# Kernel optimization log

Hardware: AMD Instinct MI355X
Metric: run time of the kernel (lower is better)

The kernel has to match this reference:

```python
import jax, jax.numpy as jnp
import numpy as np

N_TREES, N_LEAVES, PATH_LEN, N_NODES, D, B = 10, 16, 5, 31, 256, 4096


def _local_paths():
    # root-to-leaf paths of a full binary tree, depth 4: 31 nodes, 16 leaves, path len 5
    return np.array([[0, 1 + l // 8, 3 + l // 4, 7 + l // 2, 15 + l]
                     for l in range(N_LEAVES)], np.int32)


def setup_inputs() -> dict:
    key = jax.random.key(0)
    k1, k2, k3, k4, k5, k6 = jax.random.split(key, 6)
    # one activated leaf per tree -> multi-hot cross_features (B, N_TREES*N_LEAVES)
    leaf = jax.random.randint(k1, (B, N_TREES), 0, N_LEAVES)
    cross = jnp.zeros((B, N_TREES, N_LEAVES), jnp.float32)
    cross = cross.at[jnp.arange(B)[:, None], jnp.arange(N_TREES)[None, :], leaf].set(1.0)
    cross_features = cross.reshape(B, N_TREES * N_LEAVES)
    # learned params: node embedding table + single-layer LSTM (torch init scale 1/sqrt(D))
    emb = jax.random.normal(k2, (N_TREES * N_NODES, D), jnp.float32) * 0.02
    s = 1.0 / np.sqrt(D)
    W_ih = jax.random.uniform(k3, (4 * D, D), jnp.float32, -s, s)
    W_hh = jax.random.uniform(k4, (4 * D, D), jnp.float32, -s, s)
    b_ih = jax.random.uniform(k5, (4 * D,), jnp.float32, -s, s)
    b_hh = jax.random.uniform(k6, (4 * D,), jnp.float32, -s, s)
    return {"cross_features": cross_features, "emb": emb, "W_ih": W_ih,
            "W_hh": W_hh, "b_ih": b_ih, "b_hh": b_hh}


def reference(cross_features, emb, W_ih, W_hh, b_ih, b_hh):
    # global path node ids per (tree, leaf): [T, L, P]
    gpaths = jnp.asarray(_local_paths())[None, :, :] + \
        (jnp.arange(N_TREES, dtype=jnp.int32) * N_NODES)[:, None, None]
    # activated leaf per tree (exactly one hot per 16-leaf block)
    leaf = jnp.argmax(cross_features.reshape(B, N_TREES, N_LEAVES), axis=-1)  # [B, T]
    node_ids = gpaths[jnp.arange(N_TREES)[None, :], leaf]                     # [B, T, P]
    x = emb[node_ids].reshape(B * N_TREES, PATH_LEN, D)                       # packed paths
    # precompute input projections for all steps: [N, P, 4D]
    xg = jnp.einsum('npd,gd->npg', x, W_ih) + (b_ih + b_hh)

    def step(carry, xt):
        h, c = carry
        g = xt + h @ W_hh.T
        i, f, gg, o = jnp.split(g, 4, axis=-1)  # torch gate order: i, f, g, o
        c = jax.nn.sigmoid(f) * c + jax.nn.sigmoid(i) * jnp.tanh(gg)
        h = jax.nn.sigmoid(o) * jnp.tanh(c)
        return (h, c), None

    n = B * N_TREES
    h0 = jnp.zeros((n, D), x.dtype)
    (h, _), _ = jax.lax.scan(step, (h0, h0), jnp.swapaxes(xg, 0, 1))
    return h.reshape(B, N_TREES, D)
```

## Files before the change

### kernel.cpp

```cpp
#include <hip/hip_runtime.h>

#define NT 10
#define NL 16
#define NN 31
#define DD 256
#define G4 1024
#define NNODES (NT*NN)
#define NPATH (NT*NL)
#define NB 4096
#define NROWS (NB*NT)


__device__ __forceinline__ float sigf(float x)   { return 1.0f / (1.0f + __expf(-x)); }
__device__ __forceinline__ float tanh_f(float x) { return 2.0f / (1.0f + __expf(-2.0f*x)) - 1.0f; }

__global__ __launch_bounds__(256) void k_nodeproj(
    const float* __restrict__ emb, const float* __restrict__ Wih,
    const float* __restrict__ bih, const float* __restrict__ bhh,
    float* __restrict__ xg)
{
    __shared__ float smem[20 * 260 + 20 * 4 * 64];
    float4* es4 = (float4*)smem;
    float*  ps  = smem + 20 * 260;

    const int tid = threadIdx.x;
    const int nt  = blockIdx.x & 15;
    const int mt  = blockIdx.x >> 4;
    const int kq  = tid >> 6;
    const int w   = tid & 63;

    const float4* W4 = (const float4*)Wih + (size_t)(nt * 64 + w) * 64 + kq * 16;
    float4 wreg[16];
    #pragma unroll
    for (int j = 0; j < 16; ++j) wreg[j] = W4[j];

    const float4* emb4 = (const float4*)emb;
    #pragma unroll
    for (int r = 0; r < 5; ++r) {
        int idx = tid + 256 * r;
        int m = idx >> 6, q = idx & 63;
        int n = mt * 20 + m;
        es4[m * 65 + q] = (n < NNODES) ? emb4[(size_t)n * 64 + q]
                                       : make_float4(0.f, 0.f, 0.f, 0.f);
    }
    __syncthreads();

    float acc[20];
    #pragma unroll
    for (int m = 0; m < 20; ++m) acc[m] = 0.f;
    #pragma unroll
    for (int j = 0; j < 16; ++j) {
        float4 wv = wreg[j];
        #pragma unroll
        for (int m = 0; m < 20; ++m) {
            float4 h = es4[m * 65 + kq * 16 + j];
            acc[m] = fmaf(wv.x, h.x, fmaf(wv.y, h.y,
                     fmaf(wv.z, h.z, fmaf(wv.w, h.w, acc[m]))));
        }
    }
    #pragma unroll
    for (int m = 0; m < 20; ++m) ps[(m * 4 + kq) * 64 + w] = acc[m];
    __syncthreads();

    const int nl   = tid & 63;
    const int msub = tid >> 6;
    const int j    = nt * 64 + nl;
    const float bsum = bih[j] + bhh[j];
    #pragma unroll
    for (int r = 0; r < 5; ++r) {
        int m = msub * 5 + r;
        int n = mt * 20 + m;
        float s = ps[(m * 4 + 0) * 64 + nl] + ps[(m * 4 + 1) * 64 + nl]
                + ps[(m * 4 + 2) * 64 + nl] + ps[(m * 4 + 3) * 64 + nl];
        if (n < NNODES) xg[(size_t)n * G4 + j] = s + bsum;
    }
}

template<int SI, bool FIRST>
__global__ __launch_bounds__(256) void k_step(
    const float* __restrict__ xg, const float* __restrict__ Whh,
    const float* __restrict__ h_in, float* __restrict__ h_out,
    float* __restrict__ cB)
{
    __shared__ float smem[10 * 260 + 10 * 4 * 64];
    float4* hs4 = (float4*)smem;
    float*  hs  = smem;
    float*  ps  = smem + 10 * 260;

    const int tid   = threadIdx.x;
    const int pg    = blockIdx.x >> 4;
    const int dtile = blockIdx.x & 15;
    const int kq    = tid >> 6;
    const int w     = tid & 63;
    const int gate  = w >> 4;
    const int dlw   = w & 15;

    const float4* W4 = (const float4*)Whh
        + (size_t)(gate * 256 + dtile * 16 + dlw) * 64 + kq * 16;
    float4 wreg[16];
    #pragma unroll
    for (int j = 0; j < 16; ++j) wreg[j] = W4[j];

    if (FIRST) {
        #pragma unroll
        for (int r = 0; r < 10; ++r) {
            int p = r;
            int k = tid;
            int t = (pg * 10 + p) >> 4;
            const float* xr = xg + (size_t)(t * NN) * G4;
            float c1 = sigf(xr[k]) * tanh_f(xr[512 + k]);
            float h1 = sigf(xr[768 + k]) * tanh_f(c1);
            hs[p * 260 + k] = h1;
        }
    } else {
        const float4* hin4 = (const float4*)h_in;
        #pragma unroll
        for (int r = 0; r < 3; ++r) {
            int idx = tid + 256 * r;
            if (idx < 640)
                hs4[(idx >> 6) * 65 + (idx & 63)] = hin4[(size_t)pg * 640 + idx];
        }
    }
    __syncthreads();

    float acc[10];
    #pragma unroll
    for (int p = 0; p < 10; ++p) acc[p] = 0.f;
    #pragma unroll
    for (int j = 0; j < 16; ++j) {
        float4 wv = wreg[j];
        #pragma unroll
        for (int p = 0; p < 10; ++p) {
            float4 h = hs4[p * 65 + kq * 16 + j];
            acc[p] = fmaf(wv.x, h.x, fmaf(wv.y, h.y,
                     fmaf(wv.z, h.z, fmaf(wv.w, h.w, acc[p]))));
        }
    }
    #pragma unroll
    for (int p = 0; p < 10; ++p) ps[(p * 4 + kq) * 64 + w] = acc[p];
    __syncthreads();

    if (tid < 160) {
        const int p  = tid >> 4;
        const int dl = tid & 15;
        const int d  = dtile * 16 + dl;
        const int pglob = pg * 10 + p;
        const int t = pglob >> 4, l = pglob & 15;
        int off;
        if      (SI == 1) off = 1  + (l >> 3);
        else if (SI == 2) off = 3  + (l >> 2);
        else if (SI == 3) off = 7  + (l >> 1);
        else              off = 15 + l;
        const float* xn = xg + (size_t)(t * NN + off) * G4;

        float g0 = 0.f, g1 = 0.f, g2 = 0.f, g3 = 0.f;
        #pragma unroll
        for (int q = 0; q < 4; ++q) {
            g0 += ps[(p * 4 + q) * 64 +  0 + dl];
            g1 += ps[(p * 4 + q) * 64 + 16 + dl];
            g2 += ps[(p * 4 + q) * 64 + 32 + dl];
            g3 += ps[(p * 4 + q) * 64 + 48 + dl];
        }
        float c_in;
        if (FIRST) {
            int tt = pglob >> 4;
            const float* xr = xg + (size_t)(tt * NN) * G4;
            c_in = sigf(xr[d]) * tanh_f(xr[512 + d]);
        } else {
            c_in = cB[(size_t)pglob * DD + d];
        }
        float gi = g0 + xn[d];
        float gf = g1 + xn[256 + d];
        float gg = g2 + xn[512 + d];
        float go = g3 + xn[768 + d];
        float cn = sigf(gf) * c_in + sigf(gi) * tanh_f(gg);
        float hn = sigf(go) * tanh_f(cn);
        cB[(size_t)pglob * DD + d]    = cn;
        h_out[(size_t)pglob * DD + d] = hn;
    }
}

__global__ __launch_bounds__(256) void k_scatter(
    const float* __restrict__ cross, const float* __restrict__ htab,
    float* __restrict__ out)
{
    const int tid  = threadIdx.x;
    const int wave = tid >> 6;
    const int lane = tid & 63;
    const int r = blockIdx.x * 4 + wave;
    const int b = r / NT;
    const int t = r - b * NT;

    float v = 0.f;
    if (lane < NL) v = cross[(size_t)b * (NT * NL) + t * NL + lane];
    unsigned long long m = __ballot(v > 0.5f);
    int leaf = m ? (int)__builtin_ctzll(m) : 0;
    int p = t * NL + leaf;

    const float4* h4 = (const float4*)htab;
    float4* o4 = (float4*)out;
    o4[(size_t)r * 64 + lane] = h4[(size_t)p * 64 + lane];
}

extern "C" void kernel_launch(void* const* d_in, const int* in_sizes, int n_in,
                              void* d_out, int out_size, void* d_ws, size_t ws_size,
                              hipStream_t stream)
{
    const float* cross = (const float*)d_in[0];
    const float* emb   = (const float*)d_in[1];
    const float* Wih   = (const float*)d_in[2];
    const float* Whh   = (const float*)d_in[3];
    const float* bih   = (const float*)d_in[4];
    const float* bhh   = (const float*)d_in[5];
    float* out = (float*)d_out;

    float* ws = (float*)d_ws;
    float* xg = ws;
    float* hA = xg + NNODES * G4;
    float* hB = hA + NPATH * DD;
    float* cB = hB + NPATH * DD;

    hipLaunchKernelGGL(k_nodeproj, dim3(256), dim3(256), 0, stream,
                       emb, Wih, bih, bhh, xg);
    hipLaunchKernelGGL((k_step<1, true>),  dim3(256), dim3(256), 0, stream,
                       xg, Whh, hA, hA, cB);
    hipLaunchKernelGGL((k_step<2, false>), dim3(256), dim3(256), 0, stream,
                       xg, Whh, hA, hB, cB);
    hipLaunchKernelGGL((k_step<3, false>), dim3(256), dim3(256), 0, stream,
                       xg, Whh, hB, hA, cB);
    hipLaunchKernelGGL((k_step<4, false>), dim3(256), dim3(256), 0, stream,
                       xg, Whh, hA, hB, cB);
    hipLaunchKernelGGL(k_scatter, dim3(10240), dim3(256), 0, stream,
                       cross, hB, out);
}
```

Measured before the change: 125.9 us.

## Fuse node projection, LSTM steps and scatter into one cooperative kernel

Replaces the six separate launches (input projection, four recurrent steps, output gather) with a single cooperative persistent kernel of 256 blocks. Phases are separated by a hand-written grid barrier built on per-block arrival counters and a generation counter. W_hh is loaded into registers once, and the cell state stays in a register across steps instead of round-tripping through global memory. This is meant to remove launch gaps and redundant weight reloads between steps, at the cost of spin-wait barrier latency and a gather done by fewer blocks.

```diff
diff --git a/kernel.cpp b/kernel.cpp
--- a/kernel.cpp
+++ b/kernel.cpp
@@ -9,197 +9,217 @@
 #define NPATH (NT*NL)
 #define NB 4096
 #define NROWS (NB*NT)
-
+#define NBLK 256
+
+__device__ unsigned long long g_gen;
+__device__ unsigned long long g_arr[NBLK];
 
 __device__ __forceinline__ float sigf(float x)   { return 1.0f / (1.0f + __expf(-x)); }
 __device__ __forceinline__ float tanh_f(float x) { return 2.0f / (1.0f + __expf(-2.0f*x)) - 1.0f; }
 
-__global__ __launch_bounds__(256) void k_nodeproj(
-    const float* __restrict__ emb, const float* __restrict__ Wih,
-    const float* __restrict__ bih, const float* __restrict__ bhh,
-    float* __restrict__ xg)
+__device__ __forceinline__ void gbar(int bid, int tid, unsigned long long tgt,
+                                     volatile int* s_nd)
+{
+    __syncthreads();
+    if (tid == 0)
+        __hip_atomic_store(&g_arr[bid], tgt, __ATOMIC_RELEASE, __HIP_MEMORY_SCOPE_AGENT);
+    if (bid == 0) {
+        int nd = 1;
+        while (nd) {
+            if (tid == 0) *s_nd = 0;
+            __syncthreads();
+            unsigned long long v =
+                __hip_atomic_load(&g_arr[tid], __ATOMIC_RELAXED, __HIP_MEMORY_SCOPE_AGENT);
+            if (v < tgt) *s_nd = 1;
+            __syncthreads();
+            nd = *s_nd;
+            __syncthreads();
+            if (nd) __builtin_amdgcn_s_sleep(1);
+        }
+        __builtin_amdgcn_fence(__ATOMIC_ACQUIRE, "agent");
+        if (tid == 0)
+            __hip_atomic_store(&g_gen, tgt, __ATOMIC_RELEASE, __HIP_MEMORY_SCOPE_AGENT);
+    } else {
+        if (tid == 0) {
+            while (__hip_atomic_load(&g_gen, __ATOMIC_RELAXED, __HIP_MEMORY_SCOPE_AGENT) < tgt)
+                __builtin_amdgcn_s_sleep(1);
+            __builtin_amdgcn_fence(__ATOMIC_ACQUIRE, "agent");
+        }
+        __syncthreads();
+    }
+}
+
+__global__ __launch_bounds__(256) void k_fused(
+    const float* __restrict__ cross, const float* __restrict__ emb,
+    const float* __restrict__ Wih,   const float* __restrict__ Whh,
+    const float* __restrict__ bih,   const float* __restrict__ bhh,
+    float* __restrict__ out, float* __restrict__ ws)
 {
     __shared__ float smem[20 * 260 + 20 * 4 * 64];
-    float4* es4 = (float4*)smem;
-    float*  ps  = smem + 20 * 260;
+    __shared__ int s_nd;
+    __shared__ unsigned long long s_base;
+
+    float* xg = ws;
+    float* hb[2] = { xg + NNODES * G4, xg + NNODES * G4 + NPATH * DD };
 
     const int tid = threadIdx.x;
-    const int nt  = blockIdx.x & 15;
-    const int mt  = blockIdx.x >> 4;
-    const int kq  = tid >> 6;
-    const int w   = tid & 63;
-
-    const float4* W4 = (const float4*)Wih + (size_t)(nt * 64 + w) * 64 + kq * 16;
-    float4 wreg[16];
-    #pragma unroll
-    for (int j = 0; j < 16; ++j) wreg[j] = W4[j];
-
-    const float4* emb4 = (const float4*)emb;
-    #pragma unroll
-    for (int r = 0; r < 5; ++r) {
-        int idx = tid + 256 * r;
-        int m = idx >> 6, q = idx & 63;
-        int n = mt * 20 + m;
-        es4[m * 65 + q] = (n < NNODES) ? emb4[(size_t)n * 64 + q]
-                                       : make_float4(0.f, 0.f, 0.f, 0.f);
-    }
-    __syncthreads();
-
-    float acc[20];
-    #pragma unroll
-    for (int m = 0; m < 20; ++m) acc[m] = 0.f;
-    #pragma unroll
-    for (int j = 0; j < 16; ++j) {
-        float4 wv = wreg[j];
-        #pragma unroll
-        for (int m = 0; m < 20; ++m) {
-            float4 h = es4[m * 65 + kq * 16 + j];
-            acc[m] = fmaf(wv.x, h.x, fmaf(wv.y, h.y,
-                     fmaf(wv.z, h.z, fmaf(wv.w, h.w, acc[m]))));
-        }
-    }
-    #pragma unroll
-    for (int m = 0; m < 20; ++m) ps[(m * 4 + kq) * 64 + w] = acc[m];
-    __syncthreads();
-
-    const int nl   = tid & 63;
-    const int msub = tid >> 6;
-    const int j    = nt * 64 + nl;
-    const float bsum = bih[j] + bhh[j];
-    #pragma unroll
-    for (int r = 0; r < 5; ++r) {
-        int m = msub * 5 + r;
-        int n = mt * 20 + m;
-        float s = ps[(m * 4 + 0) * 64 + nl] + ps[(m * 4 + 1) * 64 + nl]
-                + ps[(m * 4 + 2) * 64 + nl] + ps[(m * 4 + 3) * 64 + nl];
-        if (n < NNODES) xg[(size_t)n * G4 + j] = s + bsum;
-    }
-}
-
-template<int SI, bool FIRST>
-__global__ __launch_bounds__(256) void k_step(
-    const float* __restrict__ xg, const float* __restrict__ Whh,
-    const float* __restrict__ h_in, float* __restrict__ h_out,
-    float* __restrict__ cB)
-{
-    __shared__ float smem[10 * 260 + 10 * 4 * 64];
-    float4* hs4 = (float4*)smem;
-    float*  hs  = smem;
-    float*  ps  = smem + 10 * 260;
-
-    const int tid   = threadIdx.x;
-    const int pg    = blockIdx.x >> 4;
-    const int dtile = blockIdx.x & 15;
-    const int kq    = tid >> 6;
-    const int w     = tid & 63;
-    const int gate  = w >> 4;
-    const int dlw   = w & 15;
-
-    const float4* W4 = (const float4*)Whh
+    const int bid = blockIdx.x;
+    if (tid == 0)
+        s_base = __hip_atomic_load(&g_gen, __ATOMIC_RELAXED, __HIP_MEMORY_SCOPE_AGENT);
+
+    {
+        float4* es4 = (float4*)smem;
+        float*  ps  = smem + 20 * 260;
+        const int nt = bid & 15, mt = bid >> 4;
+        const int kq = tid >> 6, w = tid & 63;
+        const float4* W4 = (const float4*)Wih + (size_t)(nt * 64 + w) * 64 + kq * 16;
+        float4 wr[16];
+        #pragma unroll
+        for (int j = 0; j < 16; ++j) wr[j] = W4[j];
+        const float4* emb4 = (const float4*)emb;
+        #pragma unroll
+        for (int r = 0; r < 5; ++r) {
+            int idx = tid + 256 * r;
+            int m = idx >> 6, q = idx & 63;
+            int n = mt * 20 + m;
+            es4[m * 65 + q] = (n < NNODES) ? emb4[(size_t)n * 64 + q]
+                                           : make_float4(0.f, 0.f, 0.f, 0.f);
+        }
+        __syncthreads();
+        float acc[20];
+        #pragma unroll
+        for (int m = 0; m < 20; ++m) acc[m] = 0.f;
+        #pragma unroll
+        for (int j = 0; j < 16; ++j) {
+            float4 wv = wr[j];
+            #pragma unroll
+            for (int m = 0; m < 20; ++m) {
+                float4 h = es4[m * 65 + kq * 16 + j];
+                acc[m] = fmaf(wv.x, h.x, fmaf(wv.y, h.y,
+                         fmaf(wv.z, h.z, fmaf(wv.w, h.w, acc[m]))));
+            }
+        }
+        #pragma unroll
+        for (int m = 0; m < 20; ++m) ps[(m * 4 + kq) * 64 + w] = acc[m];
+        __syncthreads();
+        const int nl   = tid & 63;
+        const int msub = tid >> 6;
+        const int j    = nt * 64 + nl;
+        const float bsum = bih[j] + bhh[j];
+        #pragma unroll
+        for (int r = 0; r < 5; ++r) {
+            int m = msub * 5 + r;
+            int n = mt * 20 + m;
+            float s = ps[(m * 4 + 0) * 64 + nl] + ps[(m * 4 + 1) * 64 + nl]
+                    + ps[(m * 4 + 2) * 64 + nl] + ps[(m * 4 + 3) * 64 + nl];
+            if (n < NNODES) xg[(size_t)n * G4 + j] = s + bsum;
+        }
+    }
+
+    const int pg    = bid >> 4;
+    const int dtile = bid & 15;
+    const int kq    = tid >> 6, w = tid & 63;
+    const int gate  = w >> 4, dlw = w & 15;
+    const float4* Wh4 = (const float4*)Whh
         + (size_t)(gate * 256 + dtile * 16 + dlw) * 64 + kq * 16;
     float4 wreg[16];
     #pragma unroll
-    for (int j = 0; j < 16; ++j) wreg[j] = W4[j];
-
-    if (FIRST) {
-        #pragma unroll
-        for (int r = 0; r < 10; ++r) {
-            int p = r;
-            int k = tid;
-            int t = (pg * 10 + p) >> 4;
-            const float* xr = xg + (size_t)(t * NN) * G4;
-            float c1 = sigf(xr[k]) * tanh_f(xr[512 + k]);
-            float h1 = sigf(xr[768 + k]) * tanh_f(c1);
-            hs[p * 260 + k] = h1;
-        }
-    } else {
-        const float4* hin4 = (const float4*)h_in;
-        #pragma unroll
-        for (int r = 0; r < 3; ++r) {
-            int idx = tid + 256 * r;
-            if (idx < 640)
-                hs4[(idx >> 6) * 65 + (idx & 63)] = hin4[(size_t)pg * 640 + idx];
-        }
-    }
-    __syncthreads();
-
-    float acc[10];
-    #pragma unroll
-    for (int p = 0; p < 10; ++p) acc[p] = 0.f;
-    #pragma unroll
-    for (int j = 0; j < 16; ++j) {
-        float4 wv = wreg[j];
-        #pragma unroll
-        for (int p = 0; p < 10; ++p) {
-            float4 h = hs4[p * 65 + kq * 16 + j];
-            acc[p] = fmaf(wv.x, h.x, fmaf(wv.y, h.y,
-                     fmaf(wv.z, h.z, fmaf(wv.w, h.w, acc[p]))));
-        }
-    }
-    #pragma unroll
-    for (int p = 0; p < 10; ++p) ps[(p * 4 + kq) * 64 + w] = acc[p];
-    __syncthreads();
-
-    if (tid < 160) {
-        const int p  = tid >> 4;
-        const int dl = tid & 15;
-        const int d  = dtile * 16 + dl;
-        const int pglob = pg * 10 + p;
-        const int t = pglob >> 4, l = pglob & 15;
-        int off;
-        if      (SI == 1) off = 1  + (l >> 3);
-        else if (SI == 2) off = 3  + (l >> 2);
-        else if (SI == 3) off = 7  + (l >> 1);
-        else              off = 15 + l;
-        const float* xn = xg + (size_t)(t * NN + off) * G4;
-
-        float g0 = 0.f, g1 = 0.f, g2 = 0.f, g3 = 0.f;
-        #pragma unroll
-        for (int q = 0; q < 4; ++q) {
-            g0 += ps[(p * 4 + q) * 64 +  0 + dl];
-            g1 += ps[(p * 4 + q) * 64 + 16 + dl];
-            g2 += ps[(p * 4 + q) * 64 + 32 + dl];
-            g3 += ps[(p * 4 + q) * 64 + 48 + dl];
-        }
-        float c_in;
-        if (FIRST) {
-            int tt = pglob >> 4;
-            const float* xr = xg + (size_t)(tt * NN) * G4;
-            c_in = sigf(xr[d]) * tanh_f(xr[512 + d]);
-        } else {
-            c_in = cB[(size_t)pglob * DD + d];
-        }
-        float gi = g0 + xn[d];
-        float gf = g1 + xn[256 + d];
-        float gg = g2 + xn[512 + d];
-        float go = g3 + xn[768 + d];
-        float cn = sigf(gf) * c_in + sigf(gi) * tanh_f(gg);
-        float hn = sigf(go) * tanh_f(cn);
-        cB[(size_t)pglob * DD + d]    = cn;
-        h_out[(size_t)pglob * DD + d] = hn;
-    }
-}
-
-__global__ __launch_bounds__(256) void k_scatter(
-    const float* __restrict__ cross, const float* __restrict__ htab,
-    float* __restrict__ out)
-{
-    const int tid  = threadIdx.x;
-    const int wave = tid >> 6;
-    const int lane = tid & 63;
-    const int r = blockIdx.x * 4 + wave;
-    const int b = r / NT;
-    const int t = r - b * NT;
-
-    float v = 0.f;
-    if (lane < NL) v = cross[(size_t)b * (NT * NL) + t * NL + lane];
-    unsigned long long m = __ballot(v > 0.5f);
-    int leaf = m ? (int)__builtin_ctzll(m) : 0;
-    int p = t * NL + leaf;
-
-    const float4* h4 = (const float4*)htab;
-    float4* o4 = (float4*)out;
-    o4[(size_t)r * 64 + lane] = h4[(size_t)p * 64 + lane];
+    for (int j = 0; j < 16; ++j) wreg[j] = Wh4[j];
+
+    gbar(bid, tid, s_base + 1, &s_nd);
+
+    {
+        float4* hs4 = (float4*)smem;
+        float*  hs  = smem;
+        float*  ps  = smem + 10 * 260;
+        const int p_act  = tid >> 4;
+        const int dl_act = tid & 15;
+        const int d_act  = dtile * 16 + dl_act;
+        const int pglob  = pg * 10 + p_act;
+        const int t_act  = pglob >> 4, l_act = pglob & 15;
+        float c_reg = 0.f;
+
+        #pragma unroll
+        for (int s = 1; s <= 4; ++s) {
+            if (s == 1) {
+                #pragma unroll
+                for (int r = 0; r < 10; ++r) {
+                    int t = (pg * 10 + r) >> 4;
+                    const float* xr = xg + (size_t)(t * NN) * G4;
+                    float c1 = sigf(xr[tid]) * tanh_f(xr[512 + tid]);
+                    hs[r * 260 + tid] = sigf(xr[768 + tid]) * tanh_f(c1);
+                }
+                if (tid < 160) {
+                    const float* xr = xg + (size_t)(t_act * NN) * G4;
+                    c_reg = sigf(xr[d_act]) * tanh_f(xr[512 + d_act]);
+                }
+            } else {
+                const float4* hin4 = (const float4*)hb[(s + 1) & 1];
+                #pragma unroll
+                for (int r = 0; r < 3; ++r) {
+                    int idx = tid + 256 * r;
+                    if (idx < 640)
+                        hs4[(idx >> 6) * 65 + (idx & 63)] = hin4[(size_t)pg * 640 + idx];
+                }
+            }
+            __syncthreads();
+
+            float acc[10];
+            #pragma unroll
+            for (int p = 0; p < 10; ++p) acc[p] = 0.f;
+            #pragma unroll
+            for (int j = 0; j < 16; ++j) {
+                float4 wv = wreg[j];
+                #pragma unroll
+                for (int p = 0; p < 10; ++p) {
+                    float4 h = hs4[p * 65 + kq * 16 + j];
+                    acc[p] = fmaf(wv.x, h.x, fmaf(wv.y, h.y,
+                             fmaf(wv.z, h.z, fmaf(wv.w, h.w, acc[p]))));
+                }
+            }
+            #pragma unroll
+            for (int p = 0; p < 10; ++p) ps[(p * 4 + kq) * 64 + w] = acc[p];
+            __syncthreads();
+
+            if (tid < 160) {
+                int off = (1 << s) - 1 + (l_act >> (4 - s));
+                const float* xn = xg + (size_t)(t_act * NN + off) * G4;
+                float g0 = 0.f, g1 = 0.f, g2 = 0.f, g3 = 0.f;
+                #pragma unroll
+                for (int q = 0; q < 4; ++q) {
+                    g0 += ps[(p_act * 4 + q) * 64 +  0 + dl_act];
+                    g1 += ps[(p_act * 4 + q) * 64 + 16 + dl_act];
+                    g2 += ps[(p_act * 4 + q) * 64 + 32 + dl_act];
+                    g3 += ps[(p_act * 4 + q) * 64 + 48 + dl_act];
+                }
+                float gi = g0 + xn[d_act];
+                float gf = g1 + xn[256 + d_act];
+                float gg = g2 + xn[512 + d_act];
+                float go = g3 + xn[768 + d_act];
+                float cn = sigf(gf) * c_reg + sigf(gi) * tanh_f(gg);
+                c_reg = cn;
+                hb[(s & 1)][(size_t)pglob * DD + d_act] = sigf(go) * tanh_f(cn);
+            }
+            gbar(bid, tid, s_base + 1 + s, &s_nd);
+        }
+    }
+
+    {
+        const int gw   = bid * 4 + (tid >> 6);
+        const int lane = tid & 63;
+        const float4* h4 = (const float4*)hb[0];
+        float4* o4 = (float4*)out;
+        for (int r = gw; r < NROWS; r += 1024) {
+            int b  = r / NT;
+            int tt = r - b * NT;
+            float v = 0.f;
+            if (lane < NL) v = cross[(size_t)b * (NT * NL) + tt * NL + lane];
+            unsigned long long m = __ballot(v > 0.5f);
+            int leaf = m ? (int)__builtin_ctzll(m) : 0;
+            int pp = tt * NL + leaf;
+            o4[(size_t)r * 64 + lane] = h4[(size_t)pp * 64 + lane];
+        }
+    }
 }
 
 extern "C" void kernel_launch(void* const* d_in, const int* in_sizes, int n_in,
@@ -213,23 +233,10 @@
     const float* bih   = (const float*)d_in[4];
     const float* bhh   = (const float*)d_in[5];
     float* out = (float*)d_out;
-
-    float* ws = (float*)d_ws;
-    float* xg = ws;
-    float* hA = xg + NNODES * G4;
-    float* hB = hA + NPATH * DD;
-    float* cB = hB + NPATH * DD;
-
-    hipLaunchKernelGGL(k_nodeproj, dim3(256), dim3(256), 0, stream,
-                       emb, Wih, bih, bhh, xg);
-    hipLaunchKernelGGL((k_step<1, true>),  dim3(256), dim3(256), 0, stream,
-                       xg, Whh, hA, hA, cB);
-    hipLaunchKernelGGL((k_step<2, false>), dim3(256), dim3(256), 0, stream,
-                       xg, Whh, hA, hB, cB);
-    hipLaunchKernelGGL((k_step<3, false>), dim3(256), dim3(256), 0, stream,
-                       xg, Whh, hB, hA, cB);
-    hipLaunchKernelGGL((k_step<4, false>), dim3(256), dim3(256), 0, stream,
-                       xg, Whh, hA, hB, cB);
-    hipLaunchKernelGGL(k_scatter, dim3(10240), dim3(256), 0, stream,
-                       cross, hB, out);
+    float* ws  = (float*)d_ws;
+
+    void* args[] = { (void*)&cross, (void*)&emb, (void*)&Wih, (void*)&Whh,
+                     (void*)&bih, (void*)&bhh, (void*)&out, (void*)&ws };
+    hipLaunchCooperativeKernel((void*)k_fused, dim3(NBLK), dim3(256),
+                               args, 0, stream);
 }
```

After: 190.8 us. +51.6%, slower.
